# Optimization experiments

Hardware: AMD Instinct MI355X
Metric: run time of the kernel (lower is better)

## Reference

```python
import jax, jax.numpy as jnp
import numpy as np

# Sampled-neighborhood cascade sizes (src->dst per layer) and edge counts
N0, N1, N2, N3 = 400000, 200000, 100000, 50000
E1, E2, E3 = 500000, 300000, 150000
DIN, DH = 128, 128


def setup_inputs() -> dict:
    key = jax.random.key(0)
    ks = jax.random.split(key, 24)
    inp = {}
    inp['x'] = jax.random.normal(ks[0], (N0, DIN), jnp.float32)
    inp['src1'] = jax.random.randint(ks[1], (E1,), 0, N0, dtype=jnp.int64)
    inp['dst1'] = jax.random.randint(ks[2], (E1,), 0, N1, dtype=jnp.int64)
    inp['src2'] = jax.random.randint(ks[3], (E2,), 0, N1, dtype=jnp.int64)
    inp['dst2'] = jax.random.randint(ks[4], (E2,), 0, N2, dtype=jnp.int64)
    inp['src3'] = jax.random.randint(ks[5], (E3,), 0, N2, dtype=jnp.int64)
    inp['dst3'] = jax.random.randint(ks[6], (E3,), 0, N3, dtype=jnp.int64)
    # SAGEConv params: lin_l (on aggregated neighbors, with bias), lin_r (root, no bias)
    dims = [(DIN, DH), (DH, DH), (DH, DH)]
    for i, (di, do) in enumerate(dims, start=1):
        s = 1.0 / np.sqrt(di)
        inp[f'Wl{i}'] = jax.random.uniform(ks[6 + 4 * i - 3], (di, do), jnp.float32, -s, s)
        inp[f'Wr{i}'] = jax.random.uniform(ks[6 + 4 * i - 2], (di, do), jnp.float32, -s, s)
        inp[f'b{i}'] = jax.random.uniform(ks[6 + 4 * i - 1], (do,), jnp.float32, -s, s)
        inp[f'a{i}'] = jnp.full((do,), 0.25, jnp.float32)  # PReLU per-channel init
    return inp


def _sage_prelu(x_src, n_dst, src, dst, Wl, Wr, b, alpha):
    # mean aggregation over incoming edges (PyG SAGEConv default aggr='mean')
    x_dst = x_src[:n_dst]                                   # [n_dst, d]
    msg = x_src[src]                                        # [E, d] gather
    summed = jax.ops.segment_sum(msg, dst, num_segments=n_dst)
    cnt = jax.ops.segment_sum(jnp.ones(src.shape[0], x_src.dtype), dst,
                              num_segments=n_dst)
    mean = summed / jnp.maximum(cnt, 1.0)[:, None]
    out = mean @ Wl + b + x_dst @ Wr                        # lin_l(aggr) + lin_r(root)
    return jnp.where(out > 0, out, alpha * out)             # per-channel PReLU


def reference(x, src1, dst1, src2, dst2, src3, dst3,
              Wl1, Wr1, b1, a1, Wl2, Wr2, b2, a2, Wl3, Wr3, b3, a3):
    h = _sage_prelu(x, N1, src1, dst1, Wl1, Wr1, b1, a1)
    h = _sage_prelu(h, N2, src2, dst2, Wl2, Wr2, b2, a2)
    h = _sage_prelu(h, N3, src3, dst3, Wl3, Wr3, b3, a3)
    return h  # [N3, DH]
```

## Files before the change

kernel.cpp:

```cpp
#include <hip/hip_runtime.h>


constexpr int cN0 = 400000, cN1 = 200000, cN2 = 100000, cN3 = 50000;
constexpr int cE1 = 500000, cE2 = 300000, cE3 = 150000;
constexpr int cNT = cN1 + cN2 + cN3;
constexpr int cET = cE1 + cE2 + cE3;

#define NDIV_UP(a, b) (((a) + (b) - 1) / (b))

typedef __attribute__((ext_vector_type(8))) short bf16x8;
typedef __attribute__((ext_vector_type(4))) float f32x4;
typedef __attribute__((ext_vector_type(4))) unsigned u32x4;

__device__ __forceinline__ unsigned fbits(float f) {
  return __builtin_bit_cast(unsigned, f);
}
__device__ __forceinline__ float ffrom(unsigned u) {
  return __builtin_bit_cast(float, u);
}
__device__ __forceinline__ unsigned short f2bf(float f) {
  unsigned u = fbits(f);
  unsigned r = u + 0x7FFFu + ((u >> 16) & 1u);
  return (unsigned short)(r >> 16);
}

__global__ void detect_idx64_kernel(const long long* __restrict__ p, int E,
                                    long long nmax, int* __restrict__ flag) {
  int t = threadIdx.x;
  int n = E < 512 ? E : 512;
  int bad = 0;
  for (int i = t; i < n; i += 64) {
    long long v = p[i];
    if (v < 0 || v >= nmax) bad = 1;
  }
  unsigned long long b = __ballot(bad);
  if (t == 0) *flag = (b == 0ull) ? 1 : 0;
}

__device__ __forceinline__ int load_idx(const void* p, int i, int flag) {
  return flag ? (int)((const long long*)p)[i] : ((const int*)p)[i];
}

constexpr int NCONV = (cN0 * 128) / 2048;
constexpr int NHIST = NDIV_UP(cET, 256);
constexpr int NPACK = NDIV_UP(3 * 16384, 256);

__global__ __launch_bounds__(256) void convhistpack_kernel(
    const float* __restrict__ x, unsigned short* __restrict__ xb,
    const void* __restrict__ d1, const void* __restrict__ d2,
    const void* __restrict__ d3, const int* __restrict__ flag,
    int* __restrict__ CNT,
    const float* __restrict__ Wl1, const float* __restrict__ Wr1,
    const float* __restrict__ Wl2, const float* __restrict__ Wr2,
    const float* __restrict__ Wl3, const float* __restrict__ Wr3,
    unsigned short* __restrict__ wpk) {
  const int bid = blockIdx.x;
  const int tid = threadIdx.x;
  if (bid < NCONV) {
    const size_t base = (size_t)bid * 2048 + tid * 8;
    const float4 v0 = *(const float4*)(x + base);
    const float4 v1 = *(const float4*)(x + base + 4);
    u32x4 o;
    o[0] = (unsigned)f2bf(v0.x) | ((unsigned)f2bf(v0.y) << 16);
    o[1] = (unsigned)f2bf(v0.z) | ((unsigned)f2bf(v0.w) << 16);
    o[2] = (unsigned)f2bf(v1.x) | ((unsigned)f2bf(v1.y) << 16);
    o[3] = (unsigned)f2bf(v1.z) | ((unsigned)f2bf(v1.w) << 16);
    *(u32x4*)(xb + base) = o;
  } else if (bid < NCONV + NHIST) {
    const int e = (bid - NCONV) * 256 + tid;
    if (e >= cET) return;
    const int f = *flag;
    int d;
    if (e < cE1) d = load_idx(d1, e, f);
    else if (e < cE1 + cE2) d = cN1 + load_idx(d2, e - cE1, f);
    else d = cN1 + cN2 + load_idx(d3, e - cE1 - cE2, f);
    atomicAdd(&CNT[d], 1);
  } else {
    const int idx = (bid - NCONV - NHIST) * 256 + tid;
    if (idx >= 3 * 16384) return;
    const int L = idx >> 14;
    const int r = idx & 16383;
    const float* Wl = L == 0 ? Wl1 : (L == 1 ? Wl2 : Wl3);
    const float* Wr = L == 0 ? Wr1 : (L == 1 ? Wr2 : Wr3);
    unsigned short* o = wpk + L * 32768;
    const int j = r & 7, l = (r >> 3) & 63, cf = (r >> 9) & 7, ks = r >> 12;
    const int k = ks * 32 + (l >> 4) * 8 + j;
    const int col = cf * 16 + (l & 15);
    o[r] = f2bf(Wl[k * 128 + col]);
    o[16384 + r] = f2bf(Wr[k * 128 + col]);
  }
}

__global__ __launch_bounds__(256) void scan_reduce(const int* __restrict__ cnt,
                                                   int n, int* __restrict__ bsum) {
  __shared__ int s[256];
  int t = threadIdx.x;
  int base = blockIdx.x * 1024 + t * 4;
  int v = 0;
  if (base + 3 < n) {
    int4 c = *(const int4*)(cnt + base);
    v = c.x + c.y + c.z + c.w;
  } else {
    for (int i = 0; i < 4; ++i)
      if (base + i < n) v += cnt[base + i];
  }
  s[t] = v;
  __syncthreads();
  for (int off = 128; off > 0; off >>= 1) {
    if (t < off) s[t] += s[t + off];
    __syncthreads();
  }
  if (t == 0) bsum[blockIdx.x] = s[0];
}

__global__ __launch_bounds__(256) void scan_bsums(int* __restrict__ bsum, int nb) {
  __shared__ int s[256];
  int t = threadIdx.x;
  int v0 = (2 * t < nb) ? bsum[2 * t] : 0;
  int v1 = (2 * t + 1 < nb) ? bsum[2 * t + 1] : 0;
  int p = v0 + v1;
  s[t] = p;
  __syncthreads();
  for (int off = 1; off < 256; off <<= 1) {
    int x = (t >= off) ? s[t - off] : 0;
    __syncthreads();
    s[t] += x;
    __syncthreads();
  }
  int excl = s[t] - p;
  if (2 * t < nb) bsum[2 * t] = excl;
  if (2 * t + 1 < nb) bsum[2 * t + 1] = excl + v0;
}

__global__ __launch_bounds__(256) void scan_final(const int* __restrict__ cnt,
                                                  int n, const int* __restrict__ bsum,
                                                  int* __restrict__ offs) {
  __shared__ int s[256];
  int t = threadIdx.x;
  int base = blockIdx.x * 1024 + t * 4;
  int v0 = 0, v1 = 0, v2 = 0, v3 = 0;
  if (base + 3 < n) {
    int4 c = *(const int4*)(cnt + base);
    v0 = c.x; v1 = c.y; v2 = c.z; v3 = c.w;
  } else {
    if (base + 0 < n) v0 = cnt[base + 0];
    if (base + 1 < n) v1 = cnt[base + 1];
    if (base + 2 < n) v2 = cnt[base + 2];
  }
  int tsum = v0 + v1 + v2 + v3;
  s[t] = tsum;
  __syncthreads();
  for (int off = 1; off < 256; off <<= 1) {
    int x = (t >= off) ? s[t - off] : 0;
    __syncthreads();
    s[t] += x;
    __syncthreads();
  }
  int excl = s[t] - tsum;
  int o = bsum[blockIdx.x] + excl;
  if (base + 0 < n) offs[base + 0] = o;
  o += v0;
  if (base + 1 < n) offs[base + 1] = o;
  o += v1;
  if (base + 2 < n) offs[base + 2] = o;
  o += v2;
  if (base + 3 < n) offs[base + 3] = o;
}

__global__ void fill3_kernel(const void* __restrict__ s1, const void* __restrict__ d1,
                             const void* __restrict__ s2, const void* __restrict__ d2,
                             const void* __restrict__ s3, const void* __restrict__ d3,
                             const int* __restrict__ flag,
                             int* __restrict__ OFFS, int* __restrict__ EID) {
  int e = blockIdx.x * 256 + threadIdx.x;
  if (e >= cET) return;
  int f = *flag;
  int s, d;
  if (e < cE1) {
    s = load_idx(s1, e, f);
    d = load_idx(d1, e, f);
  } else if (e < cE1 + cE2) {
    int i = e - cE1;
    s = load_idx(s2, i, f);
    d = cN1 + load_idx(d2, i, f);
  } else {
    int i = e - cE1 - cE2;
    s = load_idx(s3, i, f);
    d = cN1 + cN2 + load_idx(d3, i, f);
  }
  int pos = atomicAdd(&OFFS[d], 1);
  EID[pos] = s;
}

__global__ __launch_bounds__(256) void gather_kernel(
    const unsigned short* __restrict__ hsrc, const int* __restrict__ OFFS,
    const int* __restrict__ EID, int rowoff,
    unsigned short* __restrict__ meanB, int n) {
  const int wid = blockIdx.x * 4 + (threadIdx.x >> 6);
  const int lane = threadIdx.x & 63;
  const int r0 = wid * 4;
  if (r0 >= n) return;
  const int gr0 = rowoff + r0;

  int b[5];
  b[0] = (gr0 == 0) ? 0 : OFFS[gr0 - 1];
#pragma unroll
  for (int j = 0; j < 4; ++j)
    b[j + 1] = (r0 + j < n) ? OFFS[gr0 + j] : -1;
#pragma unroll
  for (int j = 0; j < 4; ++j)
    if (b[j + 1] < 0) b[j + 1] = b[j];

  float a0[4] = {0.f, 0.f, 0.f, 0.f};
  float a1[4] = {0.f, 0.f, 0.f, 0.f};

  const int bend = b[4];
  if (bend > b[0]) {
    const int blast = bend - 1;
    for (int e = b[0]; e < bend; e += 8) {
      int sid[8];
#pragma unroll
      for (int k = 0; k < 8; ++k) {
        const int ei = e + k;
        sid[k] = EID[ei <= blast ? ei : blast];
      }
      float v0[8], v1[8];
#pragma unroll
      for (int k = 0; k < 8; ++k) {
        const unsigned u = *(const unsigned*)(hsrc + (size_t)sid[k] * 128 + lane * 2);
        v0[k] = ffrom(u << 16);
        v1[k] = ffrom(u & 0xFFFF0000u);
      }
#pragma unroll
      for (int k = 0; k < 8; ++k) {
        const int ei = e + k;
#pragma unroll
        for (int j = 0; j < 4; ++j) {
          const bool p = (ei >= b[j]) & (ei < b[j + 1]);
          a0[j] += p ? v0[k] : 0.f;
          a1[j] += p ? v1[k] : 0.f;
        }
      }
    }
  }

#pragma unroll
  for (int j = 0; j < 4; ++j) {
    const int row = r0 + j;
    if (row < n) {
      const int cnt = b[j + 1] - b[j];
      const float inv = (cnt > 0) ? 1.0f / (float)cnt : 0.0f;
      const unsigned o = (unsigned)f2bf(a0[j] * inv) |
                         ((unsigned)f2bf(a1[j] * inv) << 16);
      *(unsigned*)(meanB + (size_t)row * 128 + lane * 2) = o;
    }
  }
}

template <bool OUTF32>
__global__ __launch_bounds__(256, 2) void gemm_kernel(
    const unsigned short* __restrict__ meanB,
    const unsigned short* __restrict__ xsrc,
    const unsigned short* __restrict__ W,
    const float* __restrict__ bias, const float* __restrict__ alpha,
    void* __restrict__ outp, int n) {
  __shared__ __align__(16) unsigned short wlds[32768];
  const int tid = threadIdx.x;
  const int lane = tid & 63;
  const int wv = tid >> 6;
  const int rbase = blockIdx.x * 128 + wv * 32;
  const int g = lane >> 4;
  const int r16 = lane & 15;

  bf16x8 am[2][4], ax[2][4];
#pragma unroll
  for (int t = 0; t < 2; ++t) {
    const int row = rbase + t * 16 + r16;
    const bool ok = row < n;
#pragma unroll
    for (int ks = 0; ks < 4; ++ks) {
      if (ok) {
        am[t][ks] = *(const bf16x8*)(meanB + (size_t)row * 128 + ks * 32 + g * 8);
        ax[t][ks] = *(const bf16x8*)(xsrc + (size_t)row * 128 + ks * 32 + g * 8);
      } else {
        am[t][ks] = (bf16x8)0;
        ax[t][ks] = (bf16x8)0;
      }
    }
  }

  {
    const float4* Wg = (const float4*)W;
    float4* Ws = (float4*)wlds;
#pragma unroll
    for (int i = 0; i < 16; ++i)
      Ws[i * 256 + tid] = Wg[i * 256 + tid];
  }
  __syncthreads();

  f32x4 acc[2][8] = {};
#pragma unroll
  for (int ks = 0; ks < 4; ++ks) {
    const unsigned short* wb = wlds + ks * 4096 + lane * 8;
#pragma unroll
    for (int cf = 0; cf < 8; ++cf) {
      const unsigned short* wp = wb + cf * 512;
      bf16x8 wl = *(const bf16x8*)(wp);
      bf16x8 wr = *(const bf16x8*)(wp + 16384);
#pragma unroll
      for (int t = 0; t < 2; ++t) {
        acc[t][cf] = __builtin_amdgcn_mfma_f32_16x16x32_bf16(am[t][ks], wl, acc[t][cf], 0, 0, 0);
        acc[t][cf] = __builtin_amdgcn_mfma_f32_16x16x32_bf16(ax[t][ks], wr, acc[t][cf], 0, 0, 0);
      }
    }
  }

  const int ocol0 = lane & 15;
  const int orow_off = (lane >> 4) * 4;
#pragma unroll
  for (int cf = 0; cf < 8; ++cf) {
    const int ocol = cf * 16 + ocol0;
    const float b = bias[ocol];
    const float a = alpha[ocol];
#pragma unroll
    for (int t = 0; t < 2; ++t) {
      const int orb = rbase + t * 16 + orow_off;
#pragma unroll
      for (int i = 0; i < 4; ++i) {
        const int orow = orb + i;
        if (orow < n) {
          float v = acc[t][cf][i] + b;
          v = v > 0.f ? v : a * v;
          if (OUTF32) {
            ((float*)outp)[(size_t)orow * 128 + ocol] = v;
          } else {
            ((unsigned short*)outp)[(size_t)orow * 128 + ocol] = f2bf(v);
          }
        }
      }
    }
  }
}

extern "C" void kernel_launch(void* const* d_in, const int* in_sizes, int n_in,
                              void* d_out, int out_size, void* d_ws, size_t ws_size,
                              hipStream_t stream) {
  const float* x = (const float*)d_in[0];
  const void* src1 = d_in[1];
  const void* dst1 = d_in[2];
  const void* src2 = d_in[3];
  const void* dst2 = d_in[4];
  const void* src3 = d_in[5];
  const void* dst3 = d_in[6];
  const float* Wl1 = (const float*)d_in[7];
  const float* Wr1 = (const float*)d_in[8];
  const float* b1  = (const float*)d_in[9];
  const float* a1  = (const float*)d_in[10];
  const float* Wl2 = (const float*)d_in[11];
  const float* Wr2 = (const float*)d_in[12];
  const float* b2  = (const float*)d_in[13];
  const float* a2  = (const float*)d_in[14];
  const float* Wl3 = (const float*)d_in[15];
  const float* Wr3 = (const float*)d_in[16];
  const float* b3  = (const float*)d_in[17];
  const float* a3  = (const float*)d_in[18];

  unsigned short* M1 = (unsigned short*)d_ws;
  unsigned short* xb = M1 + (size_t)cN1 * 128;
  unsigned short* M2 = xb;
  unsigned short* M3 = xb + (size_t)cN2 * 128;
  int* CNT = (int*)(xb + (size_t)cN0 * 128);
  int* OFFS = CNT + cNT;
  int* EID = OFFS + cNT;
  int* bsum = EID + cET;
  int* flag = bsum + 1024;
  unsigned short* wpk = (unsigned short*)(flag + 64);

  const int nb = NDIV_UP(cNT, 1024);

  detect_idx64_kernel<<<1, 64, 0, stream>>>((const long long*)src1, cE1,
                                            (long long)cN0, flag);
  hipMemsetAsync(CNT, 0, (size_t)cNT * sizeof(int), stream);
  convhistpack_kernel<<<NCONV + NHIST + NPACK, 256, 0, stream>>>(
      x, xb, dst1, dst2, dst3, flag, CNT,
      Wl1, Wr1, Wl2, Wr2, Wl3, Wr3, wpk);
  scan_reduce<<<nb, 256, 0, stream>>>(CNT, cNT, bsum);
  scan_bsums<<<1, 256, 0, stream>>>(bsum, nb);
  scan_final<<<nb, 256, 0, stream>>>(CNT, cNT, bsum, OFFS);
  fill3_kernel<<<NDIV_UP(cET, 256), 256, 0, stream>>>(src1, dst1, src2, dst2,
                                                      src3, dst3, flag, OFFS, EID);

  gather_kernel<<<NDIV_UP(cN1, 16), 256, 0, stream>>>(
      xb, OFFS, EID, 0, M1, cN1);
  gemm_kernel<false><<<NDIV_UP(cN1, 128), 256, 0, stream>>>(
      M1, xb, wpk, b1, a1, M1, cN1);

  gather_kernel<<<NDIV_UP(cN2, 16), 256, 0, stream>>>(
      M1, OFFS, EID, cN1, M2, cN2);
  gemm_kernel<false><<<NDIV_UP(cN2, 128), 256, 0, stream>>>(
      M2, M1, wpk + 32768, b2, a2, M2, cN2);

  gather_kernel<<<NDIV_UP(cN3, 16), 256, 0, stream>>>(
      M2, OFFS, EID, cN1 + cN2, M3, cN3);
  gemm_kernel<true><<<NDIV_UP(cN3, 128), 256, 0, stream>>>(
      M3, M2, wpk + 65536, b3, a3, d_out, cN3);
}
```

Baseline: 364.8 us.

## Split fused prep kernel and use 8-way replicated packed 16-bit histogram

The fused convert/histogram/weight-pack kernel is split into three separate kernels, and the conversion now uses a grid-stride loop. The degree histogram is spread over 8 replicas, chosen by block index, with two 16-bit counters packed into each 32-bit word, which should reduce atomic contention on hot destination rows. The scan kernels now sum the 8 replicas while reading counts. This adds extra kernel launches, an 8x larger memset and replica reads in both scan passes, and relies on per-replica counts fitting in 16 bits.

```diff
diff --git a/kernel.cpp b/kernel.cpp
--- a/kernel.cpp
+++ b/kernel.cpp
@@ -5,6 +5,7 @@
 constexpr int cE1 = 500000, cE2 = 300000, cE3 = 150000;
 constexpr int cNT = cN1 + cN2 + cN3;
 constexpr int cET = cE1 + cE2 + cE3;
+constexpr int cNTW = cNT / 2;
 
 #define NDIV_UP(a, b) (((a) + (b) - 1) / (b))
 
@@ -41,68 +42,46 @@
   return flag ? (int)((const long long*)p)[i] : ((const int*)p)[i];
 }
 
-constexpr int NCONV = (cN0 * 128) / 2048;
-constexpr int NHIST = NDIV_UP(cET, 256);
-constexpr int NPACK = NDIV_UP(3 * 16384, 256);
-
-__global__ __launch_bounds__(256) void convhistpack_kernel(
-    const float* __restrict__ x, unsigned short* __restrict__ xb,
-    const void* __restrict__ d1, const void* __restrict__ d2,
-    const void* __restrict__ d3, const int* __restrict__ flag,
-    int* __restrict__ CNT,
-    const float* __restrict__ Wl1, const float* __restrict__ Wr1,
-    const float* __restrict__ Wl2, const float* __restrict__ Wr2,
-    const float* __restrict__ Wl3, const float* __restrict__ Wr3,
-    unsigned short* __restrict__ wpk) {
-  const int bid = blockIdx.x;
-  const int tid = threadIdx.x;
-  if (bid < NCONV) {
-    const size_t base = (size_t)bid * 2048 + tid * 8;
-    const float4 v0 = *(const float4*)(x + base);
-    const float4 v1 = *(const float4*)(x + base + 4);
-    u32x4 o;
-    o[0] = (unsigned)f2bf(v0.x) | ((unsigned)f2bf(v0.y) << 16);
-    o[1] = (unsigned)f2bf(v0.z) | ((unsigned)f2bf(v0.w) << 16);
-    o[2] = (unsigned)f2bf(v1.x) | ((unsigned)f2bf(v1.y) << 16);
-    o[3] = (unsigned)f2bf(v1.z) | ((unsigned)f2bf(v1.w) << 16);
-    *(u32x4*)(xb + base) = o;
-  } else if (bid < NCONV + NHIST) {
-    const int e = (bid - NCONV) * 256 + tid;
-    if (e >= cET) return;
-    const int f = *flag;
-    int d;
-    if (e < cE1) d = load_idx(d1, e, f);
-    else if (e < cE1 + cE2) d = cN1 + load_idx(d2, e - cE1, f);
-    else d = cN1 + cN2 + load_idx(d3, e - cE1 - cE2, f);
-    atomicAdd(&CNT[d], 1);
-  } else {
-    const int idx = (bid - NCONV - NHIST) * 256 + tid;
-    if (idx >= 3 * 16384) return;
-    const int L = idx >> 14;
-    const int r = idx & 16383;
-    const float* Wl = L == 0 ? Wl1 : (L == 1 ? Wl2 : Wl3);
-    const float* Wr = L == 0 ? Wr1 : (L == 1 ? Wr2 : Wr3);
-    unsigned short* o = wpk + L * 32768;
-    const int j = r & 7, l = (r >> 3) & 63, cf = (r >> 9) & 7, ks = r >> 12;
-    const int k = ks * 32 + (l >> 4) * 8 + j;
-    const int col = cf * 16 + (l & 15);
-    o[r] = f2bf(Wl[k * 128 + col]);
-    o[16384 + r] = f2bf(Wr[k * 128 + col]);
-  }
-}
-
-__global__ __launch_bounds__(256) void scan_reduce(const int* __restrict__ cnt,
+__global__ __launch_bounds__(256) void conv_kernel(const float* __restrict__ x,
+                                                   unsigned short* __restrict__ xb) {
+  const int total4 = cN0 * 128 / 4;
+  const int stride = gridDim.x * 256;
+  for (int i = blockIdx.x * 256 + threadIdx.x; i < total4; i += stride) {
+    const float4 v = ((const float4*)x)[i];
+    uint2 o;
+    o.x = (unsigned)f2bf(v.x) | ((unsigned)f2bf(v.y) << 16);
+    o.y = (unsigned)f2bf(v.z) | ((unsigned)f2bf(v.w) << 16);
+    ((uint2*)xb)[i] = o;
+  }
+}
+
+__global__ void hist3_kernel(const void* __restrict__ d1, const void* __restrict__ d2,
+                             const void* __restrict__ d3, const int* __restrict__ flag,
+                             unsigned* __restrict__ CNT8) {
+  int e = blockIdx.x * 256 + threadIdx.x;
+  if (e >= cET) return;
+  int f = *flag;
+  int d;
+  if (e < cE1) d = load_idx(d1, e, f);
+  else if (e < cE1 + cE2) d = cN1 + load_idx(d2, e - cE1, f);
+  else d = cN1 + cN2 + load_idx(d3, e - cE1 - cE2, f);
+  atomicAdd(&CNT8[(blockIdx.x & 7) * cNTW + (d >> 1)], 1u << ((d & 1) << 4));
+}
+
+__global__ __launch_bounds__(256) void scan_reduce(const unsigned* __restrict__ CNT8,
                                                    int n, int* __restrict__ bsum) {
   __shared__ int s[256];
   int t = threadIdx.x;
   int base = blockIdx.x * 1024 + t * 4;
   int v = 0;
-  if (base + 3 < n) {
-    int4 c = *(const int4*)(cnt + base);
-    v = c.x + c.y + c.z + c.w;
-  } else {
-    for (int i = 0; i < 4; ++i)
-      if (base + i < n) v += cnt[base + i];
+  if (base < n) {
+    const int w0 = base >> 1;
+#pragma unroll
+    for (int c = 0; c < 8; ++c) {
+      const uint2 u = *(const uint2*)(CNT8 + c * cNTW + w0);
+      v += (int)(u.x & 0xFFFFu) + (int)(u.x >> 16) +
+           (int)(u.y & 0xFFFFu) + (int)(u.y >> 16);
+    }
   }
   s[t] = v;
   __syncthreads();
@@ -132,20 +111,23 @@
   if (2 * t + 1 < nb) bsum[2 * t + 1] = excl + v0;
 }
 
-__global__ __launch_bounds__(256) void scan_final(const int* __restrict__ cnt,
+__global__ __launch_bounds__(256) void scan_final(const unsigned* __restrict__ CNT8,
                                                   int n, const int* __restrict__ bsum,
                                                   int* __restrict__ offs) {
   __shared__ int s[256];
   int t = threadIdx.x;
   int base = blockIdx.x * 1024 + t * 4;
   int v0 = 0, v1 = 0, v2 = 0, v3 = 0;
-  if (base + 3 < n) {
-    int4 c = *(const int4*)(cnt + base);
-    v0 = c.x; v1 = c.y; v2 = c.z; v3 = c.w;
-  } else {
-    if (base + 0 < n) v0 = cnt[base + 0];
-    if (base + 1 < n) v1 = cnt[base + 1];
-    if (base + 2 < n) v2 = cnt[base + 2];
+  if (base < n) {
+    const int w0 = base >> 1;
+#pragma unroll
+    for (int c = 0; c < 8; ++c) {
+      const uint2 u = *(const uint2*)(CNT8 + c * cNTW + w0);
+      v0 += (int)(u.x & 0xFFFFu);
+      v1 += (int)(u.x >> 16);
+      v2 += (int)(u.y & 0xFFFFu);
+      v3 += (int)(u.y >> 16);
+    }
   }
   int tsum = v0 + v1 + v2 + v3;
   s[t] = tsum;
@@ -158,13 +140,15 @@
   }
   int excl = s[t] - tsum;
   int o = bsum[blockIdx.x] + excl;
-  if (base + 0 < n) offs[base + 0] = o;
-  o += v0;
-  if (base + 1 < n) offs[base + 1] = o;
-  o += v1;
-  if (base + 2 < n) offs[base + 2] = o;
-  o += v2;
-  if (base + 3 < n) offs[base + 3] = o;
+  if (base < n) {
+    offs[base + 0] = o;
+    o += v0;
+    offs[base + 1] = o;
+    o += v1;
+    offs[base + 2] = o;
+    o += v2;
+    offs[base + 3] = o;
+  }
 }
 
 __global__ void fill3_kernel(const void* __restrict__ s1, const void* __restrict__ d1,
@@ -190,6 +174,24 @@
   }
   int pos = atomicAdd(&OFFS[d], 1);
   EID[pos] = s;
+}
+
+__global__ void pack_w3_kernel(const float* __restrict__ Wl1, const float* __restrict__ Wr1,
+                               const float* __restrict__ Wl2, const float* __restrict__ Wr2,
+                               const float* __restrict__ Wl3, const float* __restrict__ Wr3,
+                               unsigned short* __restrict__ wpk) {
+  int idx = blockIdx.x * 256 + threadIdx.x;
+  if (idx >= 3 * 16384) return;
+  int L = idx >> 14;
+  int r = idx & 16383;
+  const float* Wl = L == 0 ? Wl1 : (L == 1 ? Wl2 : Wl3);
+  const float* Wr = L == 0 ? Wr1 : (L == 1 ? Wr2 : Wr3);
+  unsigned short* o = wpk + L * 32768;
+  int j = r & 7, l = (r >> 3) & 63, cf = (r >> 9) & 7, ks = r >> 12;
+  int k = ks * 32 + (l >> 4) * 8 + j;
+  int col = cf * 16 + (l & 15);
+  o[r] = f2bf(Wl[k * 128 + col]);
+  o[16384 + r] = f2bf(Wr[k * 128 + col]);
 }
 
 __global__ __launch_bounds__(256) void gather_kernel(
@@ -369,8 +371,8 @@
   unsigned short* xb = M1 + (size_t)cN1 * 128;
   unsigned short* M2 = xb;
   unsigned short* M3 = xb + (size_t)cN2 * 128;
-  int* CNT = (int*)(xb + (size_t)cN0 * 128);
-  int* OFFS = CNT + cNT;
+  unsigned* CNT8 = (unsigned*)(xb + (size_t)cN0 * 128);
+  int* OFFS = (int*)(CNT8 + 8 * cNTW);
   int* EID = OFFS + cNT;
   int* bsum = EID + cET;
   int* flag = bsum + 1024;
@@ -380,13 +382,13 @@
 
   detect_idx64_kernel<<<1, 64, 0, stream>>>((const long long*)src1, cE1,
                                             (long long)cN0, flag);
-  hipMemsetAsync(CNT, 0, (size_t)cNT * sizeof(int), stream);
-  convhistpack_kernel<<<NCONV + NHIST + NPACK, 256, 0, stream>>>(
-      x, xb, dst1, dst2, dst3, flag, CNT,
-      Wl1, Wr1, Wl2, Wr2, Wl3, Wr3, wpk);
-  scan_reduce<<<nb, 256, 0, stream>>>(CNT, cNT, bsum);
+  hipMemsetAsync(CNT8, 0, (size_t)8 * cNTW * sizeof(unsigned), stream);
+  conv_kernel<<<2048, 256, 0, stream>>>(x, xb);
+  pack_w3_kernel<<<192, 256, 0, stream>>>(Wl1, Wr1, Wl2, Wr2, Wl3, Wr3, wpk);
+  hist3_kernel<<<NDIV_UP(cET, 256), 256, 0, stream>>>(dst1, dst2, dst3, flag, CNT8);
+  scan_reduce<<<nb, 256, 0, stream>>>(CNT8, cNT, bsum);
   scan_bsums<<<1, 256, 0, stream>>>(bsum, nb);
-  scan_final<<<nb, 256, 0, stream>>>(CNT, cNT, bsum, OFFS);
+  scan_final<<<nb, 256, 0, stream>>>(CNT8, cNT, bsum, OFFS);
   fill3_kernel<<<NDIV_UP(cET, 256), 256, 0, stream>>>(src1, dst1, src2, dst2,
                                                       src3, dst3, flag, OFFS, EID);
 
```

New measurement: 380.9 us. 4.4% more time.
